# Kernel optimization log

Hardware: AMD Instinct MI355X
Metric: run time of the kernel (lower is better)

The kernel has to match this reference:

```python
import jax, jax.numpy as jnp
import numpy as np

P_PARTS = 6
NUM_CLASSES = 50000
BATCH = 128
PART_DIM = 256
LABEL_SMOOTH = 0.1
MARGIN = 0.3
TEMP = 3.0
KL_CLAMP = 5.0
LAMBDA_GRAPH = 0.1
LAMBDA_TRI = 1.0
LAMBDA_ADV = 0.1
START_EPOCH = 20


def setup_inputs() -> dict:
    key = jax.random.key(0)
    ks = jax.random.split(key, 8)
    id_logits = jax.random.normal(ks[0], (P_PARTS, BATCH, NUM_CLASSES), dtype=jnp.float32)
    id_features = jax.random.normal(ks[1], (P_PARTS, BATCH, PART_DIM), dtype=jnp.float32)
    gray_features = jax.random.normal(ks[2], (P_PARTS, BATCH, PART_DIM), dtype=jnp.float32)
    # soft labels are probability distributions (teacher softmax outputs)
    soft_labels = jax.nn.softmax(jax.random.normal(ks[3], (P_PARTS, BATCH, NUM_CLASSES), dtype=jnp.float32), axis=-1)
    entropy_weights = jax.random.uniform(ks[4], (P_PARTS, BATCH), dtype=jnp.float32)
    adv_logits = jax.random.normal(ks[5], (P_PARTS, BATCH, 2), dtype=jnp.float32)
    labels = jax.random.randint(ks[6], (BATCH,), 0, 16, dtype=jnp.int64 if jax.config.jax_enable_x64 else jnp.int32)
    modality_labels = jax.random.randint(ks[7], (BATCH,), 0, 2, dtype=jnp.int64 if jax.config.jax_enable_x64 else jnp.int32)
    return {
        'id_logits': id_logits,
        'id_features': id_features,
        'gray_features': gray_features,
        'soft_labels': soft_labels,
        'entropy_weights': entropy_weights,
        'adv_logits': adv_logits,
        'labels': labels,
        'modality_labels': modality_labels,
        'current_epoch': 25,
    }


def _ce(logits, labels, smoothing):
    # torch CrossEntropyLoss with label_smoothing, mean reduction. logits: [B,C]
    logp = jax.nn.log_softmax(logits, axis=-1)
    nll = -jnp.take_along_axis(logp, labels[:, None], axis=-1)[:, 0]
    smooth = -jnp.mean(logp, axis=-1)
    return jnp.mean((1.0 - smoothing) * nll + smoothing * smooth)


def _triplet(feat, target_feat, labels, same):
    # euclidean cdist [B,B]
    sq = (jnp.sum(feat * feat, axis=1)[:, None]
          + jnp.sum(target_feat * target_feat, axis=1)[None, :]
          - 2.0 * feat @ target_feat.T)
    dist = jnp.sqrt(jnp.clip(sq, 0.0) + 1e-12)
    eq = labels[:, None] == labels[None, :]
    is_neg = ~eq
    is_pos = eq & (~jnp.eye(feat.shape[0], dtype=bool)) if same else eq
    # vectorized hard mining (replaces per-row python loop)
    dist_ap = jnp.where(is_pos.any(axis=1),
                        jnp.max(jnp.where(is_pos, dist, -jnp.inf), axis=1), 0.0)
    dist_an = jnp.where(is_neg.any(axis=1),
                        jnp.min(jnp.where(is_neg, dist, jnp.inf), axis=1), 1e6)
    # MarginRankingLoss with y=1: mean(relu(dist_ap - dist_an + margin))
    return jnp.mean(jnp.maximum(dist_ap - dist_an + MARGIN, 0.0))


def reference(id_logits, id_features, gray_features, soft_labels, entropy_weights,
              adv_logits, labels, modality_labels, current_epoch):
    P = id_logits.shape[0]
    # --- multi-part ID loss ---
    L_id = jnp.mean(jax.vmap(lambda lg: _ce(lg, labels, LABEL_SMOOTH))(id_logits))
    # --- triplet on L2-normalized concatenated part features ---
    feat = jnp.concatenate(list(id_features), axis=1)  # [B, P*D]
    feat = feat / jnp.linalg.norm(feat, axis=1, keepdims=True)
    L_tri = _triplet(feat, feat, labels, same=True)
    feat_gray = jnp.concatenate(list(gray_features), axis=1)
    feat_gray = feat_gray / jnp.linalg.norm(feat_gray, axis=1, keepdims=True)
    L_trans = _triplet(feat, feat_gray, labels, same=False)
    L_tri = L_tri + 0.5 * L_trans
    # --- graph distillation (KL) ---
    if current_epoch >= START_EPOCH:
        logp = jax.nn.log_softmax(id_logits / TEMP, axis=-1)  # [P,B,C]
        kl = jnp.sum(soft_labels * (jnp.log(soft_labels) - logp), axis=-1)  # [P,B]
        kl = jnp.minimum(kl, KL_CLAMP)
        L_graph = jnp.sum(jnp.mean(kl * entropy_weights, axis=1)) * (TEMP ** 2) / P
    else:
        L_graph = jnp.float32(0.0)
    # --- adversarial CE ---
    logp_adv = jax.nn.log_softmax(adv_logits, axis=-1)  # [P,B,2]
    nll_adv = -jnp.take_along_axis(logp_adv, modality_labels[None, :, None], axis=-1)[..., 0]
    L_adv = jnp.mean(jnp.mean(nll_adv, axis=1))
    total = L_id + LAMBDA_TRI * L_tri + LAMBDA_GRAPH * L_graph + LAMBDA_ADV * L_adv
    return total
```

## Files before the change

kernel.cpp:

```cpp
#include <hip/hip_runtime.h>

#define NCLS   50000
#define NC4    12500
#define BATCH  128
#define PPARTS 6
#define NROWS  768
#define FD     1536

__device__ __forceinline__ float wave_sum(float v) {
#pragma unroll
  for (int off = 32; off > 0; off >>= 1) v += __shfl_xor(v, off, 64);
  return v;
}

__global__ void zero_k(float* acc) {
  if (threadIdx.x < 8) acc[threadIdx.x] = 0.0f;
}

__global__ __launch_bounds__(256) void big_rows_k(
    const float* __restrict__ X, const float* __restrict__ S,
    const float* __restrict__ W, const int* __restrict__ labels,
    float* __restrict__ acc) {
  const int row = blockIdx.x;
  const int b = row & (BATCH - 1);
  const int t = threadIdx.x;
  const size_t base = (size_t)row * NCLS;
  const float4* x4 = (const float4*)(X + base);
  const float4* s4 = (const float4*)(S + base);
  const float i3 = 1.0f / 3.0f;

  float x_lab = 0.0f;
  if (t == 0) x_lab = X[base + labels[b]];

  float m = -1e30f, e1 = 0.0f, e2 = 0.0f;
  float sx = 0.0f, ss = 0.0f, ssl = 0.0f, ssx = 0.0f;

  for (int i = t; i < NC4; i += 256) {
    float4 xv = x4[i];
    float4 sv = s4[i];
    float xs[4] = {xv.x, xv.y, xv.z, xv.w};
    float sc[4] = {sv.x, sv.y, sv.z, sv.w};
#pragma unroll
    for (int c = 0; c < 4; ++c) {
      float x = xs[c], s = sc[c];
      if (x > m) {
        float d = m - x;
        e1 *= __expf(d);
        e2 *= __expf(d * i3);
        m = x;
      }
      float d = x - m;
      e1 += __expf(d);
      e2 += __expf(d * i3);
      sx += x;
      ss += s;
      ssl = fmaf(s, __logf(s), ssl);
      ssx = fmaf(s, x, ssx);
    }
  }

#pragma unroll
  for (int off = 32; off > 0; off >>= 1) {
    float mo  = __shfl_xor(m, off, 64);
    float e1o = __shfl_xor(e1, off, 64);
    float e2o = __shfl_xor(e2, off, 64);
    float nm = fmaxf(m, mo);
    e1 = e1 * __expf(m - nm) + e1o * __expf(mo - nm);
    e2 = e2 * __expf((m - nm) * i3) + e2o * __expf((mo - nm) * i3);
    m = nm;
    sx  += __shfl_xor(sx, off, 64);
    ss  += __shfl_xor(ss, off, 64);
    ssl += __shfl_xor(ssl, off, 64);
    ssx += __shfl_xor(ssx, off, 64);
  }

  __shared__ float rm[4], re1[4], re2[4], rsx[4], rss[4], rssl[4], rssx[4];
  const int lane = t & 63, wid = t >> 6;
  if (lane == 0) {
    rm[wid] = m; re1[wid] = e1; re2[wid] = e2;
    rsx[wid] = sx; rss[wid] = ss; rssl[wid] = ssl; rssx[wid] = ssx;
  }
  __syncthreads();
  if (t == 0) {
    float M = rm[0], E1 = re1[0], E2 = re2[0];
#pragma unroll
    for (int wv = 1; wv < 4; ++wv) {
      float nm = fmaxf(M, rm[wv]);
      E1 = E1 * __expf(M - nm) + re1[wv] * __expf(rm[wv] - nm);
      E2 = E2 * __expf((M - nm) * i3) + re2[wv] * __expf((rm[wv] - nm) * i3);
      M = nm;
    }
    float SX  = rsx[0] + rsx[1] + rsx[2] + rsx[3];
    float SS  = rss[0] + rss[1] + rss[2] + rss[3];
    float SSL = rssl[0] + rssl[1] + rssl[2] + rssl[3];
    float SSX = rssx[0] + rssx[1] + rssx[2] + rssx[3];
    float logZ  = M + __logf(E1);
    float logZT = M * i3 + __logf(E2);
    float ce = 0.9f * (logZ - x_lab) + 0.1f * (logZ - SX * (1.0f / NCLS));
    float kl = SSL - SSX * i3 + logZT * SS;
    kl = fminf(kl, 5.0f);
    atomicAdd(&acc[0], ce);
    atomicAdd(&acc[1], kl * W[row]);
  }
}

__global__ __launch_bounds__(256) void normalize_k(
    const float* __restrict__ idf, const float* __restrict__ grayf,
    float* __restrict__ Fn, float* __restrict__ Gn) {
  const int src = blockIdx.x >> 7;
  const int b = blockIdx.x & (BATCH - 1);
  const int t = threadIdx.x;
  const float* in = src ? grayf : idf;
  float* out = src ? Gn : Fn;

  float v[6];
  float sq = 0.0f;
#pragma unroll
  for (int k = 0; k < 6; ++k) {
    v[k] = in[((k * BATCH + b) << 8) + t];
    sq = fmaf(v[k], v[k], sq);
  }
  sq = wave_sum(sq);
  __shared__ float wsum[4];
  __shared__ float inv_s;
  const int lane = t & 63, wid = t >> 6;
  if (lane == 0) wsum[wid] = sq;
  __syncthreads();
  if (t == 0) inv_s = 1.0f / sqrtf(wsum[0] + wsum[1] + wsum[2] + wsum[3]);
  __syncthreads();
  float inv = inv_s;
#pragma unroll
  for (int k = 0; k < 6; ++k)
    out[b * FD + (k << 8) + t] = v[k] * inv;
}

__global__ __launch_bounds__(256) void dist_k(
    const float* __restrict__ Fn, const float* __restrict__ Gn,
    float* __restrict__ D) {
  const int z = blockIdx.z;
  const float* Bm = z ? Gn : Fn;
  const int i0 = blockIdx.y * 16, j0 = blockIdx.x * 16;
  const int tx = threadIdx.x, ty = threadIdx.y;
  __shared__ float As[16][17], Bs[16][17];
  float acc = 0.0f;
  for (int k0 = 0; k0 < FD; k0 += 16) {
    As[ty][tx] = Fn[(i0 + ty) * FD + k0 + tx];
    Bs[ty][tx] = Bm[(j0 + ty) * FD + k0 + tx];
    __syncthreads();
#pragma unroll
    for (int k = 0; k < 16; ++k) acc = fmaf(As[ty][k], Bs[tx][k], acc);
    __syncthreads();
  }
  float sq = fmaxf(2.0f - 2.0f * acc, 0.0f) + 1e-12f;
  D[z * BATCH * BATCH + (i0 + ty) * BATCH + j0 + tx] = sqrtf(sq);
}

__global__ void mine_k(const float* __restrict__ D,
                       const int* __restrict__ labels, float* __restrict__ acc) {
  const int b = threadIdx.x;
  __shared__ int slab[BATCH];
  slab[b] = labels[b];
  __syncthreads();
  const int lb = slab[b];
  const float* d1 = D + b * BATCH;
  const float* d2 = D + BATCH * BATCH + b * BATCH;
  float ap1 = -1e30f, an1 = 1e30f, ap2 = -1e30f, an2 = 1e30f;
  int hasp1 = 0, hasn = 0, hasp2 = 0;
  for (int j = 0; j < BATCH; ++j) {
    bool eq = (slab[j] == lb);
    float v1 = d1[j], v2 = d2[j];
    if (eq) {
      hasp2 = 1; ap2 = fmaxf(ap2, v2);
      if (j != b) { hasp1 = 1; ap1 = fmaxf(ap1, v1); }
    } else {
      hasn = 1; an1 = fminf(an1, v1); an2 = fminf(an2, v2);
    }
  }
  float dap1 = hasp1 ? ap1 : 0.0f;
  float dan1 = hasn ? an1 : 1e6f;
  float l1 = fmaxf(dap1 - dan1 + 0.3f, 0.0f);
  float dap2 = hasp2 ? ap2 : 0.0f;
  float dan2 = hasn ? an2 : 1e6f;
  float l2 = fmaxf(dap2 - dan2 + 0.3f, 0.0f);
  l1 = wave_sum(l1);
  l2 = wave_sum(l2);
  __shared__ float r1[2], r2[2];
  const int lane = b & 63, wid = b >> 6;
  if (lane == 0) { r1[wid] = l1; r2[wid] = l2; }
  __syncthreads();
  if (b == 0) { acc[2] = r1[0] + r1[1]; acc[3] = r2[0] + r2[1]; }
}

__global__ void adv_k(const float* __restrict__ advl,
                      const int* __restrict__ mod, float* __restrict__ acc) {
  const int t = threadIdx.x;
  float sum = 0.0f;
#pragma unroll
  for (int k = 0; k < 3; ++k) {
    int r = t + k * 256;
    int b = r & (BATCH - 1);
    float l0 = advl[2 * r], l1 = advl[2 * r + 1];
    float mx = fmaxf(l0, l1);
    float lse = mx + __logf(__expf(l0 - mx) + __expf(l1 - mx));
    sum += lse - (mod[b] ? l1 : l0);
  }
  sum = wave_sum(sum);
  __shared__ float rs[4];
  const int lane = t & 63, wid = t >> 6;
  if (lane == 0) rs[wid] = sum;
  __syncthreads();
  if (t == 0) acc[4] = rs[0] + rs[1] + rs[2] + rs[3];
}

__global__ void fin_k(const float* __restrict__ acc,
                      const int* __restrict__ epoch, float* __restrict__ out) {
  float L_id = acc[0] * (1.0f / NROWS);
  float L_tri = acc[2] * (1.0f / BATCH) + 0.5f * acc[3] * (1.0f / BATCH);
  float L_graph = (epoch[0] >= 20) ? acc[1] * (9.0f / (6.0f * BATCH)) : 0.0f;
  float L_adv = acc[4] * (1.0f / NROWS);
  out[0] = L_id + 1.0f * L_tri + 0.1f * L_graph + 0.1f * L_adv;
}

extern "C" void kernel_launch(void* const* d_in, const int* in_sizes, int n_in,
                              void* d_out, int out_size, void* d_ws, size_t ws_size,
                              hipStream_t stream) {
  (void)in_sizes; (void)n_in; (void)out_size; (void)ws_size;
  const float* id_logits = (const float*)d_in[0];
  const float* id_feat   = (const float*)d_in[1];
  const float* gray_feat = (const float*)d_in[2];
  const float* soft      = (const float*)d_in[3];
  const float* entw      = (const float*)d_in[4];
  const float* advl      = (const float*)d_in[5];
  const int*   labels    = (const int*)d_in[6];
  const int*   modality  = (const int*)d_in[7];
  const int*   epoch     = (const int*)d_in[8];
  float* out = (float*)d_out;

  float* acc = (float*)d_ws;
  float* Fn  = acc + 16;
  float* Gn  = Fn + BATCH * FD;
  float* D   = Gn + BATCH * FD;

  zero_k<<<1, 64, 0, stream>>>(acc);
  big_rows_k<<<NROWS, 256, 0, stream>>>(id_logits, soft, entw, labels, acc);
  normalize_k<<<256, 256, 0, stream>>>(id_feat, gray_feat, Fn, Gn);
  dist_k<<<dim3(8, 8, 2), dim3(16, 16), 0, stream>>>(Fn, Gn, D);
  mine_k<<<1, BATCH, 0, stream>>>(D, labels, acc);
  adv_k<<<1, 256, 0, stream>>>(advl, modality, acc);
  fin_k<<<1, 1, 0, stream>>>(acc, epoch, out);
}
```

Before: 410.8 us.

## Split big-row reductions into chunks and fuse small tail kernels

Each of the 768 logit rows is now split into 5 chunks processed by 128-thread blocks. Each block writes partial online-softmax statistics to workspace instead of doing atomics. A single final kernel merges the partials and also performs triplet mining, the adversarial CE and the final combination, replacing four small kernels and the zeroing kernel. The goal is more parallelism and memory-level concurrency in the bandwidth-bound pass plus fewer launches, at the cost of a partial-results buffer and a serial merge in one block.

```diff
diff --git a/kernel.cpp b/kernel.cpp
--- a/kernel.cpp
+++ b/kernel.cpp
@@ -6,6 +6,8 @@
 #define PPARTS 6
 #define NROWS  768
 #define FD     1536
+#define NCHUNK 5
+#define C4     2500
 
 __device__ __forceinline__ float wave_sum(float v) {
 #pragma unroll
@@ -13,29 +15,26 @@
   return v;
 }
 
-__global__ void zero_k(float* acc) {
-  if (threadIdx.x < 8) acc[threadIdx.x] = 0.0f;
-}
-
-__global__ __launch_bounds__(256) void big_rows_k(
+__global__ __launch_bounds__(128) void chunk_k(
     const float* __restrict__ X, const float* __restrict__ S,
-    const float* __restrict__ W, const int* __restrict__ labels,
-    float* __restrict__ acc) {
-  const int row = blockIdx.x;
-  const int b = row & (BATCH - 1);
-  const int t = threadIdx.x;
+    const int* __restrict__ labels, float* __restrict__ P) {
+  const int gid = blockIdx.x;
+  const int row = gid / NCHUNK;
+  const int ch  = gid - row * NCHUNK;
+  const int b   = row & (BATCH - 1);
+  const int t   = threadIdx.x;
   const size_t base = (size_t)row * NCLS;
-  const float4* x4 = (const float4*)(X + base);
-  const float4* s4 = (const float4*)(S + base);
+  const float4* x4 = (const float4*)(X + base) + ch * C4;
+  const float4* s4 = (const float4*)(S + base) + ch * C4;
   const float i3 = 1.0f / 3.0f;
 
-  float x_lab = 0.0f;
-  if (t == 0) x_lab = X[base + labels[b]];
+  float xl = 0.0f;
+  if (ch == 0 && t == 0) xl = X[base + labels[b]];
 
   float m = -1e30f, e1 = 0.0f, e2 = 0.0f;
   float sx = 0.0f, ss = 0.0f, ssl = 0.0f, ssx = 0.0f;
 
-  for (int i = t; i < NC4; i += 256) {
+  for (int i = t; i < C4; i += 128) {
     float4 xv = x4[i];
     float4 sv = s4[i];
     float xs[4] = {xv.x, xv.y, xv.z, xv.w};
@@ -74,7 +73,7 @@
     ssx += __shfl_xor(ssx, off, 64);
   }
 
-  __shared__ float rm[4], re1[4], re2[4], rsx[4], rss[4], rssl[4], rssx[4];
+  __shared__ float rm[2], re1[2], re2[2], rsx[2], rss[2], rssl[2], rssx[2];
   const int lane = t & 63, wid = t >> 6;
   if (lane == 0) {
     rm[wid] = m; re1[wid] = e1; re2[wid] = e2;
@@ -83,24 +82,14 @@
   __syncthreads();
   if (t == 0) {
     float M = rm[0], E1 = re1[0], E2 = re2[0];
-#pragma unroll
-    for (int wv = 1; wv < 4; ++wv) {
-      float nm = fmaxf(M, rm[wv]);
-      E1 = E1 * __expf(M - nm) + re1[wv] * __expf(rm[wv] - nm);
-      E2 = E2 * __expf((M - nm) * i3) + re2[wv] * __expf((rm[wv] - nm) * i3);
-      M = nm;
-    }
-    float SX  = rsx[0] + rsx[1] + rsx[2] + rsx[3];
-    float SS  = rss[0] + rss[1] + rss[2] + rss[3];
-    float SSL = rssl[0] + rssl[1] + rssl[2] + rssl[3];
-    float SSX = rssx[0] + rssx[1] + rssx[2] + rssx[3];
-    float logZ  = M + __logf(E1);
-    float logZT = M * i3 + __logf(E2);
-    float ce = 0.9f * (logZ - x_lab) + 0.1f * (logZ - SX * (1.0f / NCLS));
-    float kl = SSL - SSX * i3 + logZT * SS;
-    kl = fminf(kl, 5.0f);
-    atomicAdd(&acc[0], ce);
-    atomicAdd(&acc[1], kl * W[row]);
+    float nm = fmaxf(M, rm[1]);
+    E1 = E1 * __expf(M - nm) + re1[1] * __expf(rm[1] - nm);
+    E2 = E2 * __expf((M - nm) * i3) + re2[1] * __expf((rm[1] - nm) * i3);
+    M = nm;
+    float4* o = (float4*)(P + (size_t)gid * 8);
+    o[0] = make_float4(M, E1, E2, rsx[0] + rsx[1]);
+    o[1] = make_float4(rss[0] + rss[1], rssl[0] + rssl[1],
+                       rssx[0] + rssx[1], xl);
   }
 }
 
@@ -155,70 +144,99 @@
   D[z * BATCH * BATCH + (i0 + ty) * BATCH + j0 + tx] = sqrtf(sq);
 }
 
-__global__ void mine_k(const float* __restrict__ D,
-                       const int* __restrict__ labels, float* __restrict__ acc) {
-  const int b = threadIdx.x;
+__global__ __launch_bounds__(256) void final_k(
+    const float* __restrict__ P, const float* __restrict__ W,
+    const float* __restrict__ D, const float* __restrict__ advl,
+    const int* __restrict__ labels, const int* __restrict__ mod,
+    const int* __restrict__ epoch, float* __restrict__ out) {
+  const int t = threadIdx.x;
+  const float i3 = 1.0f / 3.0f;
   __shared__ int slab[BATCH];
-  slab[b] = labels[b];
-  __syncthreads();
-  const int lb = slab[b];
-  const float* d1 = D + b * BATCH;
-  const float* d2 = D + BATCH * BATCH + b * BATCH;
-  float ap1 = -1e30f, an1 = 1e30f, ap2 = -1e30f, an2 = 1e30f;
-  int hasp1 = 0, hasn = 0, hasp2 = 0;
-  for (int j = 0; j < BATCH; ++j) {
-    bool eq = (slab[j] == lb);
-    float v1 = d1[j], v2 = d2[j];
-    if (eq) {
-      hasp2 = 1; ap2 = fmaxf(ap2, v2);
-      if (j != b) { hasp1 = 1; ap1 = fmaxf(ap1, v1); }
-    } else {
-      hasn = 1; an1 = fminf(an1, v1); an2 = fminf(an2, v2);
+  if (t < BATCH) slab[t] = labels[t];
+
+  float ce = 0.0f, klw = 0.0f;
+#pragma unroll
+  for (int k = 0; k < 3; ++k) {
+    const int row = t + k * 256;
+    const float* p = P + (size_t)row * NCHUNK * 8;
+    float M = p[0], E1 = p[1], E2 = p[2], SX = p[3];
+    float SS = p[4], SSL = p[5], SSX = p[6];
+    const float xl = p[7];
+#pragma unroll
+    for (int ch = 1; ch < NCHUNK; ++ch) {
+      const float* q = p + ch * 8;
+      float mo = q[0];
+      float nm = fmaxf(M, mo);
+      E1 = E1 * __expf(M - nm) + q[1] * __expf(mo - nm);
+      E2 = E2 * __expf((M - nm) * i3) + q[2] * __expf((mo - nm) * i3);
+      M = nm;
+      SX += q[3]; SS += q[4]; SSL += q[5]; SSX += q[6];
     }
-  }
-  float dap1 = hasp1 ? ap1 : 0.0f;
-  float dan1 = hasn ? an1 : 1e6f;
-  float l1 = fmaxf(dap1 - dan1 + 0.3f, 0.0f);
-  float dap2 = hasp2 ? ap2 : 0.0f;
-  float dan2 = hasn ? an2 : 1e6f;
-  float l2 = fmaxf(dap2 - dan2 + 0.3f, 0.0f);
-  l1 = wave_sum(l1);
-  l2 = wave_sum(l2);
-  __shared__ float r1[2], r2[2];
-  const int lane = b & 63, wid = b >> 6;
-  if (lane == 0) { r1[wid] = l1; r2[wid] = l2; }
-  __syncthreads();
-  if (b == 0) { acc[2] = r1[0] + r1[1]; acc[3] = r2[0] + r2[1]; }
-}
-
-__global__ void adv_k(const float* __restrict__ advl,
-                      const int* __restrict__ mod, float* __restrict__ acc) {
-  const int t = threadIdx.x;
-  float sum = 0.0f;
+    float logZ  = M + __logf(E1);
+    float logZT = M * i3 + __logf(E2);
+    ce += 0.9f * (logZ - xl) + 0.1f * (logZ - SX * (1.0f / NCLS));
+    float kl = SSL - SSX * i3 + logZT * SS;
+    klw += fminf(kl, 5.0f) * W[row];
+  }
+
+  float adv = 0.0f;
 #pragma unroll
   for (int k = 0; k < 3; ++k) {
-    int r = t + k * 256;
-    int b = r & (BATCH - 1);
+    const int r = t + k * 256;
+    const int b = r & (BATCH - 1);
     float l0 = advl[2 * r], l1 = advl[2 * r + 1];
     float mx = fmaxf(l0, l1);
     float lse = mx + __logf(__expf(l0 - mx) + __expf(l1 - mx));
-    sum += lse - (mod[b] ? l1 : l0);
-  }
-  sum = wave_sum(sum);
-  __shared__ float rs[4];
+    adv += lse - (mod[b] ? l1 : l0);
+  }
+
+  __syncthreads();
+  float l1s = 0.0f, l2s = 0.0f;
+  if (t < BATCH) {
+    const int lb = slab[t];
+    const float* d1 = D + t * BATCH;
+    const float* d2 = D + BATCH * BATCH + t * BATCH;
+    float ap1 = -1e30f, an1 = 1e30f, ap2 = -1e30f, an2 = 1e30f;
+    int hasp1 = 0, hasn = 0, hasp2 = 0;
+    for (int j = 0; j < BATCH; ++j) {
+      bool eq = (slab[j] == lb);
+      float v1 = d1[j], v2 = d2[j];
+      if (eq) {
+        hasp2 = 1; ap2 = fmaxf(ap2, v2);
+        if (j != t) { hasp1 = 1; ap1 = fmaxf(ap1, v1); }
+      } else {
+        hasn = 1; an1 = fminf(an1, v1); an2 = fminf(an2, v2);
+      }
+    }
+    float dap1 = hasp1 ? ap1 : 0.0f;
+    float dan1 = hasn ? an1 : 1e6f;
+    l1s = fmaxf(dap1 - dan1 + 0.3f, 0.0f);
+    float dap2 = hasp2 ? ap2 : 0.0f;
+    float dan2 = hasn ? an2 : 1e6f;
+    l2s = fmaxf(dap2 - dan2 + 0.3f, 0.0f);
+  }
+
+  ce  = wave_sum(ce);
+  klw = wave_sum(klw);
+  adv = wave_sum(adv);
+  l1s = wave_sum(l1s);
+  l2s = wave_sum(l2s);
+  __shared__ float r0[4], r1[4], r2[4], r3[4], r4[4];
   const int lane = t & 63, wid = t >> 6;
-  if (lane == 0) rs[wid] = sum;
-  __syncthreads();
-  if (t == 0) acc[4] = rs[0] + rs[1] + rs[2] + rs[3];
-}
-
-__global__ void fin_k(const float* __restrict__ acc,
-                      const int* __restrict__ epoch, float* __restrict__ out) {
-  float L_id = acc[0] * (1.0f / NROWS);
-  float L_tri = acc[2] * (1.0f / BATCH) + 0.5f * acc[3] * (1.0f / BATCH);
-  float L_graph = (epoch[0] >= 20) ? acc[1] * (9.0f / (6.0f * BATCH)) : 0.0f;
-  float L_adv = acc[4] * (1.0f / NROWS);
-  out[0] = L_id + 1.0f * L_tri + 0.1f * L_graph + 0.1f * L_adv;
+  if (lane == 0) { r0[wid]=ce; r1[wid]=klw; r2[wid]=adv; r3[wid]=l1s; r4[wid]=l2s; }
+  __syncthreads();
+  if (t == 0) {
+    float CE  = r0[0] + r0[1] + r0[2] + r0[3];
+    float KLW = r1[0] + r1[1] + r1[2] + r1[3];
+    float ADV = r2[0] + r2[1] + r2[2] + r2[3];
+    float T1  = r3[0] + r3[1] + r3[2] + r3[3];
+    float T2  = r4[0] + r4[1] + r4[2] + r4[3];
+    float L_id    = CE * (1.0f / NROWS);
+    float L_tri   = (T1 + 0.5f * T2) * (1.0f / BATCH);
+    float L_graph = (epoch[0] >= 20) ? KLW * (9.0f / 768.0f) : 0.0f;
+    float L_adv   = ADV * (1.0f / NROWS);
+    out[0] = L_id + L_tri + 0.1f * L_graph + 0.1f * L_adv;
+  }
 }
 
 extern "C" void kernel_launch(void* const* d_in, const int* in_sizes, int n_in,
@@ -236,16 +254,13 @@
   const int*   epoch     = (const int*)d_in[8];
   float* out = (float*)d_out;
 
-  float* acc = (float*)d_ws;
-  float* Fn  = acc + 16;
-  float* Gn  = Fn + BATCH * FD;
-  float* D   = Gn + BATCH * FD;
-
-  zero_k<<<1, 64, 0, stream>>>(acc);
-  big_rows_k<<<NROWS, 256, 0, stream>>>(id_logits, soft, entw, labels, acc);
+  float* P  = (float*)d_ws;
+  float* Fn = P + NROWS * NCHUNK * 8;
+  float* Gn = Fn + BATCH * FD;
+  float* D  = Gn + BATCH * FD;
+
+  chunk_k<<<NROWS * NCHUNK, 128, 0, stream>>>(id_logits, soft, labels, P);
   normalize_k<<<256, 256, 0, stream>>>(id_feat, gray_feat, Fn, Gn);
   dist_k<<<dim3(8, 8, 2), dim3(16, 16), 0, stream>>>(Fn, Gn, D);
-  mine_k<<<1, BATCH, 0, stream>>>(D, labels, acc);
-  adv_k<<<1, 256, 0, stream>>>(advl, modality, acc);
-  fin_k<<<1, 1, 0, stream>>>(acc, epoch, out);
-}
+  final_k<<<1, 256, 0, stream>>>(P, entw, D, advl, labels, modality, epoch, out);
+}
```

New measurement: 406.1 us. No clear change (-1.2%).
